# Kernel tuning notes

Hardware: AMD Instinct MI355X
Metric: run time of the kernel (lower is better)

The kernel has to match this reference:

```python
import math
import jax, jax.numpy as jnp
import numpy as np

B, S, D = 4, 2048, 1024
L = 2                      # codec_decoder_transformer_lengths entry
H, HD = 8, 128             # n_heads == n_kv_heads (no GQA repeat)
FF = 4096
WINDOW = 16                # sliding window (causal: keys in [i-16, i])
NORM_EPS = 0.01
QK_EPS = 1e-6
SCALE_INIT = 0.1           # layer_id < 18 -> 0.1


def _alibi_slopes(n):
    # n is a power of 2 here (8)
    r = 2.0 ** (-8.0 / n)
    return jnp.array([r ** (i + 1) for i in range(n)], dtype=jnp.float32)


def rms_norm(x, w, eps):
    return x * jax.lax.rsqrt(jnp.mean(x * x, axis=-1, keepdims=True) + eps) * w


def _attn_bias(dtype):
    pos = jnp.arange(S)
    rel = pos[None, :] - pos[:, None]          # [S,S], rel = j - i
    slopes = _alibi_slopes(H).astype(dtype)
    bias = slopes[:, None, None] * rel[None].astype(dtype)   # [H,S,S]
    mask = (rel > 0) | (rel < -WINDOW)         # causal + sliding window
    return jnp.where(mask[None], -jnp.inf, bias)


def setup_inputs() -> dict:
    key = jax.random.key(0)
    ks = jax.random.split(key, 9)
    sd = 0.02
    w = lambda k, shape: jax.random.normal(k, shape, jnp.float32) * sd
    return {
        "x": jax.random.normal(ks[0], (B, S, D), jnp.float32),
        "wq": w(ks[1], (L, D, H * HD)),
        "wk": w(ks[2], (L, D, H * HD)),
        "wv": w(ks[3], (L, D, H * HD)),
        "wo": w(ks[4], (L, H * HD, D)),
        "q_norm_w": jnp.ones((L, H * HD), jnp.float32),
        "k_norm_w": jnp.ones((L, H * HD), jnp.float32),
        "w1": w(ks[5], (L, D, FF)),
        "w2": w(ks[6], (L, FF, D)),
        "w3": w(ks[7], (L, D, FF)),
        "attn_norm_w": jnp.ones((L, D), jnp.float32),
        "ffn_norm_w": jnp.ones((L, D), jnp.float32),
        "attn_scale": jnp.full((L, D), SCALE_INIT, jnp.float32),
        "ffn_scale": jnp.full((L, D), SCALE_INIT, jnp.float32),
    }


def reference(x, wq, wk, wv, wo, q_norm_w, k_norm_w, w1, w2, w3,
              attn_norm_w, ffn_norm_w, attn_scale, ffn_scale):
    bias = _attn_bias(x.dtype)                 # [H,S,S]
    inv_sqrt_d = 1.0 / math.sqrt(HD)

    def block(h, p):
        (lwq, lwk, lwv, lwo, qnw, knw, lw1, lw2, lw3, anw, fnw, asc, fsc) = p
        xn = rms_norm(h, anw, NORM_EPS)
        # qk_norm applied on the flat (H*HD) projection before the head split
        q = rms_norm(xn @ lwq, qnw, QK_EPS).reshape(B, S, H, HD).transpose(0, 2, 1, 3)
        k = rms_norm(xn @ lwk, knw, QK_EPS).reshape(B, S, H, HD).transpose(0, 2, 1, 3)
        v = (xn @ lwv).reshape(B, S, H, HD).transpose(0, 2, 1, 3)
        scores = jnp.einsum('bhqd,bhkd->bhqk', q, k) * inv_sqrt_d + bias[None]
        attn = jax.nn.softmax(scores, axis=-1)
        y = jnp.einsum('bhqk,bhkd->bhqd', attn, v)
        y = y.transpose(0, 2, 1, 3).reshape(B, S, H * HD)
        h = h + asc * (y @ lwo)
        xn = rms_norm(h, fnw, NORM_EPS)
        ff = (jax.nn.silu(xn @ lw1) * (xn @ lw3)) @ lw2
        return h + fsc * ff, None

    out, _ = jax.lax.scan(
        block, x,
        (wq, wk, wv, wo, q_norm_w, k_norm_w, w1, w2, w3,
         attn_norm_w, ffn_norm_w, attn_scale, ffn_scale))
    return out
```

## Files before the change

kernel.cpp:

```cpp
#include <hip/hip_runtime.h>

#define B_ 4
#define S_ 2048
#define D_ 1024
#define H_ 8
#define HD_ 128
#define FF_ 4096
#define R_ (B_*S_)

typedef __attribute__((ext_vector_type(8))) short short8;
typedef __attribute__((ext_vector_type(4))) float f32x4;

__device__ __forceinline__ unsigned short f2bf(float f) {
  unsigned int u = __float_as_uint(f);
  return (unsigned short)((u + 0x7fffu + ((u >> 16) & 1u)) >> 16);
}
__device__ __forceinline__ float bf2f(unsigned short s) {
  return __uint_as_float(((unsigned int)s) << 16);
}

typedef const __attribute__((address_space(1))) unsigned int* gas_p;
typedef __attribute__((address_space(3))) unsigned int* las_p;
__device__ __forceinline__ void gload16(const void* g, void* l) {
  __builtin_amdgcn_global_load_lds((gas_p)g, (las_p)l, 16, 0, 0);
}

__global__ __launch_bounds__(256) void f2bf_t(const float* __restrict__ src,
    unsigned short* __restrict__ dst, int Rows, int Cols) {
  __shared__ float tile[32][33];
  const int tx = threadIdx.x & 31, ty = threadIdx.x >> 5;
  const int r0 = blockIdx.y * 32, c0 = blockIdx.x * 32;
  #pragma unroll
  for (int j = 0; j < 32; j += 8)
    tile[ty + j][tx] = src[(size_t)(r0 + ty + j) * Cols + c0 + tx];
  __syncthreads();
  #pragma unroll
  for (int j = 0; j < 32; j += 8)
    dst[(size_t)(c0 + ty + j) * Rows + r0 + tx] = f2bf(tile[tx][ty + j]);
}

__global__ __launch_bounds__(256) void rmsnorm_f2b(const float* __restrict__ in,
    const float* __restrict__ w, unsigned short* __restrict__ out, float eps) {
  const int row = blockIdx.x, t = threadIdx.x;
  const float4 xv = *(const float4*)&in[(size_t)row * D_ + t * 4];
  float p = xv.x*xv.x + xv.y*xv.y + xv.z*xv.z + xv.w*xv.w;
  #pragma unroll
  for (int off = 32; off >= 1; off >>= 1) p += __shfl_xor(p, off);
  __shared__ float red[4];
  if ((t & 63) == 0) red[t >> 6] = p;
  __syncthreads();
  float scl = rsqrtf((red[0] + red[1] + red[2] + red[3]) * (1.0f / D_) + eps);
  const float4 wv = *(const float4*)&w[t * 4];
  ((ushort4*)out)[(size_t)row * 256 + t] = make_ushort4(
      f2bf(xv.x*scl*wv.x), f2bf(xv.y*scl*wv.y), f2bf(xv.z*scl*wv.z), f2bf(xv.w*scl*wv.w));
}

__global__ __launch_bounds__(256) void qknorm_k(unsigned short* __restrict__ qkv,
    const float* __restrict__ qw, const float* __restrict__ kw) {
  const int row = blockIdx.x, t = threadIdx.x;
  unsigned short* qp = qkv + (size_t)row * 3072;
  unsigned short* kp = qp + 1024;
  const ushort4 qv = ((const ushort4*)qp)[t];
  const ushort4 kv = ((const ushort4*)kp)[t];
  float q0 = bf2f(qv.x), q1 = bf2f(qv.y), q2 = bf2f(qv.z), q3 = bf2f(qv.w);
  float k0 = bf2f(kv.x), k1 = bf2f(kv.y), k2 = bf2f(kv.z), k3 = bf2f(kv.w);
  float pq = q0*q0 + q1*q1 + q2*q2 + q3*q3;
  float pk = k0*k0 + k1*k1 + k2*k2 + k3*k3;
  #pragma unroll
  for (int off = 32; off >= 1; off >>= 1) { pq += __shfl_xor(pq, off); pk += __shfl_xor(pk, off); }
  __shared__ float redq[4], redk[4];
  if ((t & 63) == 0) { redq[t >> 6] = pq; redk[t >> 6] = pk; }
  __syncthreads();
  float sq = rsqrtf((redq[0]+redq[1]+redq[2]+redq[3]) * (1.0f / D_) + 1e-6f);
  float sk = rsqrtf((redk[0]+redk[1]+redk[2]+redk[3]) * (1.0f / D_) + 1e-6f);
  const float4 qwv = *(const float4*)&qw[t * 4];
  const float4 kwv = *(const float4*)&kw[t * 4];
  ((ushort4*)qp)[t] = make_ushort4(f2bf(q0*sq*qwv.x), f2bf(q1*sq*qwv.y),
                                   f2bf(q2*sq*qwv.z), f2bf(q3*sq*qwv.w));
  ((ushort4*)kp)[t] = make_ushort4(f2bf(k0*sk*kwv.x), f2bf(k1*sk*kwv.y),
                                   f2bf(k2*sk*kwv.z), f2bf(k3*sk*kwv.w));
}

__global__ __launch_bounds__(256) void attn_k(const unsigned short* __restrict__ qkv,
    unsigned short* __restrict__ y) {
  const int lane = threadIdx.x & 63;
  const int wid = (blockIdx.x * 256 + threadIdx.x) >> 6;
  const int i  = wid & (S_ - 1);
  const int bh = wid >> 11;
  const int hh = bh & (H_ - 1);
  const int b  = bh >> 3;
  const float slope = exp2f(-(float)(hh + 1));
  const float inv = 0.088388347648318447f;
  const size_t rowq = ((size_t)(b * S_ + i)) * 3072 + hh * HD_ + lane * 2;
  const ushort2 qv = *(const ushort2*)&qkv[rowq];
  const float qx = bf2f(qv.x), qy = bf2f(qv.y);
  float sc[17];
  #pragma unroll
  for (int jj = 0; jj < 17; ++jj) {
    int j = i - 16 + jj;
    int jc = j < 0 ? 0 : j;
    size_t koff = ((size_t)(b * S_ + jc)) * 3072 + 1024 + hh * HD_ + lane * 2;
    ushort2 kv = *(const ushort2*)&qkv[koff];
    float p = qx * bf2f(kv.x) + qy * bf2f(kv.y);
    p += __shfl_xor(p, 32); p += __shfl_xor(p, 16); p += __shfl_xor(p, 8);
    p += __shfl_xor(p, 4);  p += __shfl_xor(p, 2);  p += __shfl_xor(p, 1);
    sc[jj] = (j >= 0) ? (p * inv + slope * (float)(jj - 16)) : -1e30f;
  }
  float m = sc[0];
  #pragma unroll
  for (int jj = 1; jj < 17; ++jj) m = fmaxf(m, sc[jj]);
  float wsum = 0.f, ax = 0.f, ay = 0.f;
  #pragma unroll
  for (int jj = 0; jj < 17; ++jj) {
    int j = i - 16 + jj;
    int jc = j < 0 ? 0 : j;
    float wgt = expf(sc[jj] - m);
    size_t voff = ((size_t)(b * S_ + jc)) * 3072 + 2048 + hh * HD_ + lane * 2;
    ushort2 vv = *(const ushort2*)&qkv[voff];
    wsum += wgt; ax += wgt * bf2f(vv.x); ay += wgt * bf2f(vv.y);
  }
  float rs = 1.f / wsum;
  size_t yoff = ((size_t)(b * S_ + i)) * 1024 + hh * HD_ + lane * 2;
  *(ushort2*)&y[yoff] = make_ushort2(f2bf(ax * rs), f2bf(ay * rs));
}


__device__ __forceinline__ void stage_tile(const unsigned short* __restrict__ src,
    unsigned short* lds, int rowbase, int K, int k0, int t) {
  #pragma unroll
  for (int it = 0; it < 4; ++it) {
    int g = it * 256 + t;
    int row = g >> 3, slot = g & 7;
    int sc8 = (slot ^ (row & 7)) << 3;
    gload16(&src[(size_t)(rowbase + row) * K + k0 + sc8], &lds[g * 8]);
  }
}

__global__ __launch_bounds__(256, 2) void gemm_tn(
    const unsigned short* __restrict__ A, const unsigned short* __restrict__ Bt,
    unsigned short* __restrict__ C, int M, int N, int K) {
  __shared__ __align__(16) unsigned short As[128 * 64];
  __shared__ __align__(16) unsigned short Bs[128 * 64];
  const int t = threadIdx.x;
  const int lane = t & 63, w = t >> 6;
  const int wr = w >> 1, wc = w & 1;
  const int br = blockIdx.y * 128, bc = blockIdx.x * 128;
  const int lr = lane & 15, lk = lane >> 4;
  const int xm = lr & 7;
  f32x4 acc[4][4];
  #pragma unroll
  for (int mi = 0; mi < 4; ++mi)
    #pragma unroll
    for (int ni = 0; ni < 4; ++ni) { f32x4 z = {0.f,0.f,0.f,0.f}; acc[mi][ni] = z; }
  for (int k0 = 0; k0 < K; k0 += 64) {
    stage_tile(A,  As, br, K, k0, t);
    stage_tile(Bt, Bs, bc, K, k0, t);
    __syncthreads();
    #pragma unroll
    for (int kk = 0; kk < 2; ++kk) {
      short8 af[4], bfr[4];
      #pragma unroll
      for (int mi = 0; mi < 4; ++mi)
        af[mi] = *(const short8*)&As[(wr*64 + mi*16 + lr) * 64 + (((kk*4 + lk) ^ xm) << 3)];
      #pragma unroll
      for (int ni = 0; ni < 4; ++ni)
        bfr[ni] = *(const short8*)&Bs[(wc*64 + ni*16 + lr) * 64 + (((kk*4 + lk) ^ xm) << 3)];
      #pragma unroll
      for (int mi = 0; mi < 4; ++mi)
        #pragma unroll
        for (int ni = 0; ni < 4; ++ni)
          acc[mi][ni] = __builtin_amdgcn_mfma_f32_16x16x32_bf16(af[mi], bfr[ni], acc[mi][ni], 0, 0, 0);
    }
    __syncthreads();
  }
  #pragma unroll
  for (int mi = 0; mi < 4; ++mi)
    #pragma unroll
    for (int ni = 0; ni < 4; ++ni) {
      int row = br + wr * 64 + mi * 16 + lk * 4;
      int col = bc + wc * 64 + ni * 16 + lr;
      #pragma unroll
      for (int r = 0; r < 4; ++r)
        C[(size_t)(row + r) * N + col] = f2bf(acc[mi][ni][r]);
    }
}

__global__ __launch_bounds__(256, 2) void gemm_ep(
    const unsigned short* __restrict__ A, const unsigned short* __restrict__ Bt,
    float* __restrict__ h, const float* __restrict__ sc, int M, int N, int K) {
  __shared__ __align__(16) unsigned short As[128 * 64];
  __shared__ __align__(16) unsigned short Bs[128 * 64];
  const int t = threadIdx.x;
  const int lane = t & 63, w = t >> 6;
  const int wr = w >> 1, wc = w & 1;
  const int br = blockIdx.y * 128, bc = blockIdx.x * 128;
  const int lr = lane & 15, lk = lane >> 4;
  const int xm = lr & 7;
  f32x4 acc[4][4];
  #pragma unroll
  for (int mi = 0; mi < 4; ++mi)
    #pragma unroll
    for (int ni = 0; ni < 4; ++ni) { f32x4 z = {0.f,0.f,0.f,0.f}; acc[mi][ni] = z; }
  for (int k0 = 0; k0 < K; k0 += 64) {
    stage_tile(A,  As, br, K, k0, t);
    stage_tile(Bt, Bs, bc, K, k0, t);
    __syncthreads();
    #pragma unroll
    for (int kk = 0; kk < 2; ++kk) {
      short8 af[4], bfr[4];
      #pragma unroll
      for (int mi = 0; mi < 4; ++mi)
        af[mi] = *(const short8*)&As[(wr*64 + mi*16 + lr) * 64 + (((kk*4 + lk) ^ xm) << 3)];
      #pragma unroll
      for (int ni = 0; ni < 4; ++ni)
        bfr[ni] = *(const short8*)&Bs[(wc*64 + ni*16 + lr) * 64 + (((kk*4 + lk) ^ xm) << 3)];
      #pragma unroll
      for (int mi = 0; mi < 4; ++mi)
        #pragma unroll
        for (int ni = 0; ni < 4; ++ni)
          acc[mi][ni] = __builtin_amdgcn_mfma_f32_16x16x32_bf16(af[mi], bfr[ni], acc[mi][ni], 0, 0, 0);
    }
    __syncthreads();
  }
  #pragma unroll
  for (int ni = 0; ni < 4; ++ni) {
    int col = bc + wc * 64 + ni * 16 + lr;
    float sv = sc[col];
    #pragma unroll
    for (int mi = 0; mi < 4; ++mi) {
      int row = br + wr * 64 + mi * 16 + lk * 4;
      #pragma unroll
      for (int r = 0; r < 4; ++r)
        h[(size_t)(row + r) * N + col] += sv * acc[mi][ni][r];
    }
  }
}

__global__ __launch_bounds__(256, 2) void gemm_w13(
    const unsigned short* __restrict__ A, const unsigned short* __restrict__ B1t,
    const unsigned short* __restrict__ B3t, unsigned short* __restrict__ G,
    int M, int N, int K) {
  __shared__ __align__(16) unsigned short As[128 * 64];
  __shared__ __align__(16) unsigned short B1s[128 * 64];
  __shared__ __align__(16) unsigned short B3s[128 * 64];
  const int t = threadIdx.x;
  const int lane = t & 63, w = t >> 6;
  const int wr = w >> 1, wc = w & 1;
  const int br = blockIdx.y * 128, bc = blockIdx.x * 128;
  const int lr = lane & 15, lk = lane >> 4;
  const int xm = lr & 7;
  f32x4 acc1[4][4], acc3[4][4];
  #pragma unroll
  for (int mi = 0; mi < 4; ++mi)
    #pragma unroll
    for (int ni = 0; ni < 4; ++ni) {
      f32x4 z = {0.f,0.f,0.f,0.f}; acc1[mi][ni] = z; acc3[mi][ni] = z;
    }
  for (int k0 = 0; k0 < K; k0 += 64) {
    stage_tile(A,   As,  br, K, k0, t);
    stage_tile(B1t, B1s, bc, K, k0, t);
    stage_tile(B3t, B3s, bc, K, k0, t);
    __syncthreads();
    #pragma unroll
    for (int kk = 0; kk < 2; ++kk) {
      short8 af[4], b1r[4], b3r[4];
      #pragma unroll
      for (int mi = 0; mi < 4; ++mi)
        af[mi] = *(const short8*)&As[(wr*64 + mi*16 + lr) * 64 + (((kk*4 + lk) ^ xm) << 3)];
      #pragma unroll
      for (int ni = 0; ni < 4; ++ni) {
        b1r[ni] = *(const short8*)&B1s[(wc*64 + ni*16 + lr) * 64 + (((kk*4 + lk) ^ xm) << 3)];
        b3r[ni] = *(const short8*)&B3s[(wc*64 + ni*16 + lr) * 64 + (((kk*4 + lk) ^ xm) << 3)];
      }
      #pragma unroll
      for (int mi = 0; mi < 4; ++mi)
        #pragma unroll
        for (int ni = 0; ni < 4; ++ni) {
          acc1[mi][ni] = __builtin_amdgcn_mfma_f32_16x16x32_bf16(af[mi], b1r[ni], acc1[mi][ni], 0, 0, 0);
          acc3[mi][ni] = __builtin_amdgcn_mfma_f32_16x16x32_bf16(af[mi], b3r[ni], acc3[mi][ni], 0, 0, 0);
        }
    }
    __syncthreads();
  }
  #pragma unroll
  for (int mi = 0; mi < 4; ++mi)
    #pragma unroll
    for (int ni = 0; ni < 4; ++ni) {
      int row = br + wr * 64 + mi * 16 + lk * 4;
      int col = bc + wc * 64 + ni * 16 + lr;
      #pragma unroll
      for (int r = 0; r < 4; ++r) {
        float a1 = acc1[mi][ni][r], a3 = acc3[mi][ni][r];
        G[(size_t)(row + r) * N + col] = f2bf(a1 / (1.f + expf(-a1)) * a3);
      }
    }
}

extern "C" void kernel_launch(void* const* d_in, const int* in_sizes, int n_in,
                              void* d_out, int out_size, void* d_ws, size_t ws_size,
                              hipStream_t stream) {
  const float* x    = (const float*)d_in[0];
  const float* wq   = (const float*)d_in[1];
  const float* wk   = (const float*)d_in[2];
  const float* wv   = (const float*)d_in[3];
  const float* wo   = (const float*)d_in[4];
  const float* qnw  = (const float*)d_in[5];
  const float* knw  = (const float*)d_in[6];
  const float* w1   = (const float*)d_in[7];
  const float* w2   = (const float*)d_in[8];
  const float* w3   = (const float*)d_in[9];
  const float* anw  = (const float*)d_in[10];
  const float* fnw  = (const float*)d_in[11];
  const float* asc  = (const float*)d_in[12];
  const float* fsc  = (const float*)d_in[13];

  const size_t MB = 1024 * 1024;
  if (ws_size < 144 * MB) return;

  float* h = (float*)d_out;
  char* ws = (char*)d_ws;
  unsigned short* qkvt = (unsigned short*)ws;
  unsigned short* wot  = qkvt + 2u * 3145728u;
  unsigned short* w1t  = wot  + 2u * 1048576u;
  unsigned short* w3t  = w1t  + 2u * 4194304u;
  unsigned short* w2t  = w3t  + 2u * 4194304u;
  unsigned short* xn   = (unsigned short*)(ws + 64 * MB);
  unsigned short* qkv  = (unsigned short*)(ws + 80 * MB);
  unsigned short* gate = qkv;

  hipMemcpyAsync(h, x, (size_t)R_ * D_ * sizeof(float), hipMemcpyDeviceToDevice, stream);

  for (int l = 0; l < 2; ++l) {
    unsigned short* qkvt_l = qkvt + (size_t)l * 3145728u;
    f2bf_t<<<dim3(32, 32),  256, 0, stream>>>(wq + (size_t)l*1048576, qkvt_l,            1024, 1024);
    f2bf_t<<<dim3(32, 32),  256, 0, stream>>>(wk + (size_t)l*1048576, qkvt_l + 1048576,  1024, 1024);
    f2bf_t<<<dim3(32, 32),  256, 0, stream>>>(wv + (size_t)l*1048576, qkvt_l + 2097152,  1024, 1024);
    f2bf_t<<<dim3(32, 32),  256, 0, stream>>>(wo + (size_t)l*1048576, wot + (size_t)l*1048576, 1024, 1024);
    f2bf_t<<<dim3(128, 32), 256, 0, stream>>>(w1 + (size_t)l*4194304, w1t + (size_t)l*4194304, 1024, 4096);
    f2bf_t<<<dim3(128, 32), 256, 0, stream>>>(w3 + (size_t)l*4194304, w3t + (size_t)l*4194304, 1024, 4096);
    f2bf_t<<<dim3(32, 128), 256, 0, stream>>>(w2 + (size_t)l*4194304, w2t + (size_t)l*4194304, 4096, 1024);
  }

  for (int l = 0; l < 2; ++l) {
    rmsnorm_f2b<<<R_, 256, 0, stream>>>(h, anw + l * D_, xn, 0.01f);
    gemm_tn<<<dim3(24, 64), 256, 0, stream>>>(xn, qkvt + (size_t)l*3145728u, qkv, R_, 3072, 1024);
    qknorm_k<<<R_, 256, 0, stream>>>(qkv, qnw + l * 1024, knw + l * 1024);
    attn_k<<<R_ * H_ / 4, 256, 0, stream>>>(qkv, xn);
    gemm_ep<<<dim3(8, 64), 256, 0, stream>>>(xn, wot + (size_t)l*1048576u, h, asc + l * D_,
                                             R_, 1024, 1024);
    rmsnorm_f2b<<<R_, 256, 0, stream>>>(h, fnw + l * D_, xn, 0.01f);
    gemm_w13<<<dim3(32, 64), 256, 0, stream>>>(xn, w1t + (size_t)l*4194304u,
                                               w3t + (size_t)l*4194304u, gate, R_, 4096, 1024);
    gemm_ep<<<dim3(8, 64), 256, 0, stream>>>(gate, w2t + (size_t)l*4194304u, h, fsc + l * D_,
                                             R_, 1024, 4096);
  }
}
```

Measured before the change: 910.5 us.

## Replace 128x128 GEMMs with double-buffered 256x256 pipelined MFMA kernel

Adds a templated 256x256-tile GEMM with 8 waves, double-buffered LDS, interleaved global-to-LDS prefetch of the next K tile across four MFMA quadrants, s_setprio scheduling, and a grouped block swizzle for L2 reuse. It replaces the QKV, output-projection and w2 GEMMs. The aim is to hide memory latency and raise arithmetic intensity per block. The cost is heavier register pressure and fewer blocks: 128 blocks for the N=1024 GEMMs, which is below the CU count and may underfill the device.

```diff
diff --git a/kernel.cpp b/kernel.cpp
--- a/kernel.cpp
+++ b/kernel.cpp
@@ -124,6 +124,180 @@
   *(ushort2*)&y[yoff] = make_ushort2(f2bf(ax * rs), f2bf(ay * rs));
 }
 
+template<int EPI>
+__global__ __launch_bounds__(512, 2) void gemm256(
+    const unsigned short* __restrict__ A, const unsigned short* __restrict__ Bt,
+    void* __restrict__ Cout, const float* __restrict__ sc, int M, int N, int K) {
+  __shared__ __align__(16) unsigned short lds[2][2][16384];
+  const int t = threadIdx.x;
+  const int lane = t & 63, w = t >> 6;
+  const int wm = w >> 2, wn = w & 3;
+  const int lr = lane & 15, lk = lane >> 4;
+  const int xm = lr & 7;
+
+  const int nbx = N >> 8;
+  const int nwg = gridDim.x;
+  const int bid = blockIdx.x;
+  const int swz = (bid & 7) * (nwg >> 3) + (bid >> 3);
+  const int br = (swz / nbx) << 8;
+  const int bc = (swz % nbx) << 8;
+
+  const unsigned short* Abase = A + (size_t)br * K;
+  const unsigned short* Bbase = Bt + (size_t)bc * K;
+
+  auto stageA = [&](int buf, int u, int k0) {
+    #pragma unroll
+    for (int j = 0; j < 2; ++j) {
+      int gr = (t + (j << 9)) >> 3, slot = t & 7;
+      int row = ((gr & 63) | ((gr >> 6) << 7)) + (u << 6);
+      gload16(Abase + (size_t)row * K + k0 + ((slot ^ (row & 7)) << 3),
+              &lds[buf][0][row * 64 + slot * 8]);
+    }
+  };
+  auto stageB = [&](int buf, int u, int k0) {
+    #pragma unroll
+    for (int j = 0; j < 2; ++j) {
+      int gr = (t + (j << 9)) >> 3, slot = t & 7;
+      int row = ((gr & 31) | ((gr >> 5) << 6)) + (u << 5);
+      gload16(Bbase + (size_t)row * K + k0 + ((slot ^ (row & 7)) << 3),
+              &lds[buf][1][row * 64 + slot * 8]);
+    }
+  };
+
+  f32x4 acc[8][4];
+  #pragma unroll
+  for (int mi = 0; mi < 8; ++mi)
+    #pragma unroll
+    for (int ni = 0; ni < 4; ++ni) { f32x4 z = {0.f,0.f,0.f,0.f}; acc[mi][ni] = z; }
+
+  const int NT = K >> 6;
+  stageA(0, 0, 0); stageB(0, 0, 0); stageA(0, 1, 0); stageB(0, 1, 0);
+  asm volatile("s_waitcnt vmcnt(0)" ::: "memory");
+  __builtin_amdgcn_s_barrier();
+
+  for (int kt = 0; kt < NT; ++kt) {
+    const int cur = kt & 1, nxt = cur ^ 1;
+    const int kp = (kt + 1 < NT) ? ((kt + 1) << 6) : 0;
+    const unsigned short* Al = lds[cur][0];
+    const unsigned short* Bl = lds[cur][1];
+    short8 af[4][2], bfA[2][2], bfB[2][2];
+
+    #pragma unroll
+    for (int mf = 0; mf < 4; ++mf)
+      #pragma unroll
+      for (int ks = 0; ks < 2; ++ks)
+        af[mf][ks] = *(const short8*)&Al[(wm*128 + mf*16 + lr)*64 + (((ks*4+lk)^xm)<<3)];
+    #pragma unroll
+    for (int nf = 0; nf < 2; ++nf)
+      #pragma unroll
+      for (int ks = 0; ks < 2; ++ks)
+        bfA[nf][ks] = *(const short8*)&Bl[(wn*64 + nf*16 + lr)*64 + (((ks*4+lk)^xm)<<3)];
+    stageA(nxt, 0, kp);
+    asm volatile("s_waitcnt vmcnt(2)" ::: "memory");
+    __builtin_amdgcn_s_barrier();
+    asm volatile("s_waitcnt lgkmcnt(0)" ::: "memory");
+    __builtin_amdgcn_sched_barrier(0);
+    __builtin_amdgcn_s_setprio(1);
+    #pragma unroll
+    for (int mf = 0; mf < 4; ++mf)
+      #pragma unroll
+      for (int nf = 0; nf < 2; ++nf)
+        #pragma unroll
+        for (int ks = 0; ks < 2; ++ks)
+          acc[mf][nf] = __builtin_amdgcn_mfma_f32_16x16x32_bf16(af[mf][ks], bfA[nf][ks], acc[mf][nf], 0, 0, 0);
+    __builtin_amdgcn_s_setprio(0);
+    __builtin_amdgcn_s_barrier();
+
+    #pragma unroll
+    for (int nf = 0; nf < 2; ++nf)
+      #pragma unroll
+      for (int ks = 0; ks < 2; ++ks)
+        bfB[nf][ks] = *(const short8*)&Bl[(wn*64 + (nf+2)*16 + lr)*64 + (((ks*4+lk)^xm)<<3)];
+    stageB(nxt, 0, kp);
+    __builtin_amdgcn_s_barrier();
+    asm volatile("s_waitcnt lgkmcnt(0)" ::: "memory");
+    __builtin_amdgcn_sched_barrier(0);
+    __builtin_amdgcn_s_setprio(1);
+    #pragma unroll
+    for (int mf = 0; mf < 4; ++mf)
+      #pragma unroll
+      for (int nf = 0; nf < 2; ++nf)
+        #pragma unroll
+        for (int ks = 0; ks < 2; ++ks)
+          acc[mf][nf+2] = __builtin_amdgcn_mfma_f32_16x16x32_bf16(af[mf][ks], bfB[nf][ks], acc[mf][nf+2], 0, 0, 0);
+    __builtin_amdgcn_s_setprio(0);
+    __builtin_amdgcn_s_barrier();
+
+    #pragma unroll
+    for (int mf = 0; mf < 4; ++mf)
+      #pragma unroll
+      for (int ks = 0; ks < 2; ++ks)
+        af[mf][ks] = *(const short8*)&Al[(wm*128 + (mf+4)*16 + lr)*64 + (((ks*4+lk)^xm)<<3)];
+    stageA(nxt, 1, kp);
+    __builtin_amdgcn_s_barrier();
+    asm volatile("s_waitcnt lgkmcnt(0)" ::: "memory");
+    __builtin_amdgcn_sched_barrier(0);
+    __builtin_amdgcn_s_setprio(1);
+    #pragma unroll
+    for (int mf = 0; mf < 4; ++mf)
+      #pragma unroll
+      for (int nf = 0; nf < 2; ++nf)
+        #pragma unroll
+        for (int ks = 0; ks < 2; ++ks)
+          acc[mf+4][nf+2] = __builtin_amdgcn_mfma_f32_16x16x32_bf16(af[mf][ks], bfB[nf][ks], acc[mf+4][nf+2], 0, 0, 0);
+    __builtin_amdgcn_s_setprio(0);
+    __builtin_amdgcn_s_barrier();
+
+    #pragma unroll
+    for (int nf = 0; nf < 2; ++nf)
+      #pragma unroll
+      for (int ks = 0; ks < 2; ++ks)
+        bfA[nf][ks] = *(const short8*)&Bl[(wn*64 + nf*16 + lr)*64 + (((ks*4+lk)^xm)<<3)];
+    stageB(nxt, 1, kp);
+    asm volatile("s_waitcnt vmcnt(4)" ::: "memory");
+    __builtin_amdgcn_s_barrier();
+    asm volatile("s_waitcnt lgkmcnt(0)" ::: "memory");
+    __builtin_amdgcn_sched_barrier(0);
+    __builtin_amdgcn_s_setprio(1);
+    #pragma unroll
+    for (int mf = 0; mf < 4; ++mf)
+      #pragma unroll
+      for (int nf = 0; nf < 2; ++nf)
+        #pragma unroll
+        for (int ks = 0; ks < 2; ++ks)
+          acc[mf+4][nf] = __builtin_amdgcn_mfma_f32_16x16x32_bf16(af[mf][ks], bfA[nf][ks], acc[mf+4][nf], 0, 0, 0);
+    __builtin_amdgcn_s_setprio(0);
+    __builtin_amdgcn_s_barrier();
+  }
+
+  if (EPI == 0) {
+    unsigned short* C = (unsigned short*)Cout;
+    #pragma unroll
+    for (int mf = 0; mf < 8; ++mf)
+      #pragma unroll
+      for (int nf = 0; nf < 4; ++nf) {
+        int row = br + wm*128 + mf*16 + lk*4;
+        int col = bc + wn*64 + nf*16 + lr;
+        #pragma unroll
+        for (int r = 0; r < 4; ++r)
+          C[(size_t)(row + r) * N + col] = f2bf(acc[mf][nf][r]);
+      }
+  } else {
+    float* hp = (float*)Cout;
+    #pragma unroll
+    for (int nf = 0; nf < 4; ++nf) {
+      int col = bc + wn*64 + nf*16 + lr;
+      float sv = sc[col];
+      #pragma unroll
+      for (int mf = 0; mf < 8; ++mf) {
+        int row = br + wm*128 + mf*16 + lk*4;
+        #pragma unroll
+        for (int r = 0; r < 4; ++r)
+          hp[(size_t)(row + r) * N + col] += sv * acc[mf][nf][r];
+      }
+    }
+  }
+}
 
 __device__ __forceinline__ void stage_tile(const unsigned short* __restrict__ src,
     unsigned short* lds, int rowbase, int K, int k0, int t) {
@@ -133,106 +307,6 @@
     int row = g >> 3, slot = g & 7;
     int sc8 = (slot ^ (row & 7)) << 3;
     gload16(&src[(size_t)(rowbase + row) * K + k0 + sc8], &lds[g * 8]);
-  }
-}
-
-__global__ __launch_bounds__(256, 2) void gemm_tn(
-    const unsigned short* __restrict__ A, const unsigned short* __restrict__ Bt,
-    unsigned short* __restrict__ C, int M, int N, int K) {
-  __shared__ __align__(16) unsigned short As[128 * 64];
-  __shared__ __align__(16) unsigned short Bs[128 * 64];
-  const int t = threadIdx.x;
-  const int lane = t & 63, w = t >> 6;
-  const int wr = w >> 1, wc = w & 1;
-  const int br = blockIdx.y * 128, bc = blockIdx.x * 128;
-  const int lr = lane & 15, lk = lane >> 4;
-  const int xm = lr & 7;
-  f32x4 acc[4][4];
-  #pragma unroll
-  for (int mi = 0; mi < 4; ++mi)
-    #pragma unroll
-    for (int ni = 0; ni < 4; ++ni) { f32x4 z = {0.f,0.f,0.f,0.f}; acc[mi][ni] = z; }
-  for (int k0 = 0; k0 < K; k0 += 64) {
-    stage_tile(A,  As, br, K, k0, t);
-    stage_tile(Bt, Bs, bc, K, k0, t);
-    __syncthreads();
-    #pragma unroll
-    for (int kk = 0; kk < 2; ++kk) {
-      short8 af[4], bfr[4];
-      #pragma unroll
-      for (int mi = 0; mi < 4; ++mi)
-        af[mi] = *(const short8*)&As[(wr*64 + mi*16 + lr) * 64 + (((kk*4 + lk) ^ xm) << 3)];
-      #pragma unroll
-      for (int ni = 0; ni < 4; ++ni)
-        bfr[ni] = *(const short8*)&Bs[(wc*64 + ni*16 + lr) * 64 + (((kk*4 + lk) ^ xm) << 3)];
-      #pragma unroll
-      for (int mi = 0; mi < 4; ++mi)
-        #pragma unroll
-        for (int ni = 0; ni < 4; ++ni)
-          acc[mi][ni] = __builtin_amdgcn_mfma_f32_16x16x32_bf16(af[mi], bfr[ni], acc[mi][ni], 0, 0, 0);
-    }
-    __syncthreads();
-  }
-  #pragma unroll
-  for (int mi = 0; mi < 4; ++mi)
-    #pragma unroll
-    for (int ni = 0; ni < 4; ++ni) {
-      int row = br + wr * 64 + mi * 16 + lk * 4;
-      int col = bc + wc * 64 + ni * 16 + lr;
-      #pragma unroll
-      for (int r = 0; r < 4; ++r)
-        C[(size_t)(row + r) * N + col] = f2bf(acc[mi][ni][r]);
-    }
-}
-
-__global__ __launch_bounds__(256, 2) void gemm_ep(
-    const unsigned short* __restrict__ A, const unsigned short* __restrict__ Bt,
-    float* __restrict__ h, const float* __restrict__ sc, int M, int N, int K) {
-  __shared__ __align__(16) unsigned short As[128 * 64];
-  __shared__ __align__(16) unsigned short Bs[128 * 64];
-  const int t = threadIdx.x;
-  const int lane = t & 63, w = t >> 6;
-  const int wr = w >> 1, wc = w & 1;
-  const int br = blockIdx.y * 128, bc = blockIdx.x * 128;
-  const int lr = lane & 15, lk = lane >> 4;
-  const int xm = lr & 7;
-  f32x4 acc[4][4];
-  #pragma unroll
-  for (int mi = 0; mi < 4; ++mi)
-    #pragma unroll
-    for (int ni = 0; ni < 4; ++ni) { f32x4 z = {0.f,0.f,0.f,0.f}; acc[mi][ni] = z; }
-  for (int k0 = 0; k0 < K; k0 += 64) {
-    stage_tile(A,  As, br, K, k0, t);
-    stage_tile(Bt, Bs, bc, K, k0, t);
-    __syncthreads();
-    #pragma unroll
-    for (int kk = 0; kk < 2; ++kk) {
-      short8 af[4], bfr[4];
-      #pragma unroll
-      for (int mi = 0; mi < 4; ++mi)
-        af[mi] = *(const short8*)&As[(wr*64 + mi*16 + lr) * 64 + (((kk*4 + lk) ^ xm) << 3)];
-      #pragma unroll
-      for (int ni = 0; ni < 4; ++ni)
-        bfr[ni] = *(const short8*)&Bs[(wc*64 + ni*16 + lr) * 64 + (((kk*4 + lk) ^ xm) << 3)];
-      #pragma unroll
-      for (int mi = 0; mi < 4; ++mi)
-        #pragma unroll
-        for (int ni = 0; ni < 4; ++ni)
-          acc[mi][ni] = __builtin_amdgcn_mfma_f32_16x16x32_bf16(af[mi], bfr[ni], acc[mi][ni], 0, 0, 0);
-    }
-    __syncthreads();
-  }
-  #pragma unroll
-  for (int ni = 0; ni < 4; ++ni) {
-    int col = bc + wc * 64 + ni * 16 + lr;
-    float sv = sc[col];
-    #pragma unroll
-    for (int mi = 0; mi < 4; ++mi) {
-      int row = br + wr * 64 + mi * 16 + lk * 4;
-      #pragma unroll
-      for (int r = 0; r < 4; ++r)
-        h[(size_t)(row + r) * N + col] += sv * acc[mi][ni][r];
-    }
   }
 }
 
@@ -343,15 +417,16 @@
 
   for (int l = 0; l < 2; ++l) {
     rmsnorm_f2b<<<R_, 256, 0, stream>>>(h, anw + l * D_, xn, 0.01f);
-    gemm_tn<<<dim3(24, 64), 256, 0, stream>>>(xn, qkvt + (size_t)l*3145728u, qkv, R_, 3072, 1024);
+    gemm256<0><<<384, 512, 0, stream>>>(xn, qkvt + (size_t)l*3145728u, qkv, nullptr,
+                                        R_, 3072, 1024);
     qknorm_k<<<R_, 256, 0, stream>>>(qkv, qnw + l * 1024, knw + l * 1024);
     attn_k<<<R_ * H_ / 4, 256, 0, stream>>>(qkv, xn);
-    gemm_ep<<<dim3(8, 64), 256, 0, stream>>>(xn, wot + (size_t)l*1048576u, h, asc + l * D_,
-                                             R_, 1024, 1024);
+    gemm256<1><<<128, 512, 0, stream>>>(xn, wot + (size_t)l*1048576u, h, asc + l * D_,
+                                        R_, 1024, 1024);
     rmsnorm_f2b<<<R_, 256, 0, stream>>>(h, fnw + l * D_, xn, 0.01f);
     gemm_w13<<<dim3(32, 64), 256, 0, stream>>>(xn, w1t + (size_t)l*4194304u,
                                                w3t + (size_t)l*4194304u, gate, R_, 4096, 1024);
-    gemm_ep<<<dim3(8, 64), 256, 0, stream>>>(gate, w2t + (size_t)l*4194304u, h, fsc + l * D_,
-                                             R_, 1024, 4096);
-  }
-}
+    gemm256<1><<<128, 512, 0, stream>>>(gate, w2t + (size_t)l*4194304u, h, fsc + l * D_,
+                                        R_, 1024, 4096);
+  }
+}
```

Result: slower. 1.016 ms (+11.6%).
